# Kernel optimization log

Measured on AMD Instinct MI355X. Metric: run time of the kernel, lower is better.

## Reference

```python
import jax, jax.numpy as jnp
import numpy as np

B, S, D, H = 2, 2048, 1024, 16
DH = D // H


def setup_inputs() -> dict:
    key = jax.random.key(0)
    ks = jax.random.split(key, 13)
    def lin(kw, kb):
        w = jax.random.normal(kw, (D, D), dtype=jnp.float32) * (1.0 / np.sqrt(D))
        b = jax.random.normal(kb, (D,), dtype=jnp.float32) * 0.01
        return w, b
    wq_w, wq_b = lin(ks[0], ks[1])
    wk_w, wk_b = lin(ks[2], ks[3])
    wv_w, wv_b = lin(ks[4], ks[5])
    dense_w, dense_b = lin(ks[6], ks[7])
    q = jax.random.normal(ks[8], (B, S, D), dtype=jnp.float32)
    k = jax.random.normal(ks[9], (B, S, D), dtype=jnp.float32)
    v = jax.random.normal(ks[10], (B, S, D), dtype=jnp.float32)
    mask = jax.random.randint(ks[11], (B, 1, S, S), 0, 2, dtype=jnp.int32)
    return {"q": q, "k": k, "v": v, "mask": mask,
            "wq_w": wq_w, "wq_b": wq_b, "wk_w": wk_w, "wk_b": wk_b,
            "wv_w": wv_w, "wv_b": wv_b, "dense_w": dense_w, "dense_b": dense_b}


def _split_heads(x):
    # [B,S,D] -> [B,H,S,DH]
    b, s, _ = x.shape
    return x.reshape(b, s, H, DH).transpose(0, 2, 1, 3)


def reference(q, k, v, mask, wq_w, wq_b, wk_w, wk_b, wv_w, wv_b, dense_w, dense_b):
    qs = _split_heads(q @ wq_w.T + wq_b)
    ks = _split_heads(k @ wk_w.T + wk_b)
    vs = _split_heads(v @ wv_w.T + wv_b)
    scale = 1.0 / np.sqrt(float(DH))
    scores = jnp.einsum('bhqd,bhkd->bhqk', qs, ks) * scale  # [B,H,S,S]
    scores = jnp.where(mask == 0, -jnp.inf, scores)
    weights = jax.nn.softmax(scores, axis=-1)
    out = jnp.einsum('bhqk,bhkd->bhqd', weights, vs)
    out = out.transpose(0, 2, 1, 3).reshape(q.shape[0], -1, D)  # merge heads
    out = out @ dense_w.T + dense_b
    return (out, weights)
```

## Files before the change

kernel.cpp:

```cpp
#include <hip/hip_runtime.h>
#include <math.h>

#define Bb 2
#define Ss 2048
#define Dd 1024
#define Hh 16
#define DHh 64

typedef unsigned short u16;
typedef unsigned int u32;
typedef __attribute__((ext_vector_type(8))) short short8;
typedef __attribute__((ext_vector_type(4))) float f32x4;

#define LOG2E 1.44269504088896340736f

__device__ __forceinline__ u16 fb(float f){
    u32 x = __float_as_uint(f);
    return (u16)((x + 0x7fffu + ((x>>16)&1u)) >> 16);
}
__device__ __forceinline__ float bf2f(u16 h){
    return __uint_as_float((u32)h << 16);
}

__global__ __launch_bounds__(256) void split_hilo(
    const float* __restrict__ x, u16* __restrict__ hi, u16* __restrict__ lo,
    int n8)
{
    const int i = blockIdx.x*256 + threadIdx.x;
    if (i >= n8) return;
    float4 a = ((const float4*)x)[i*2];
    float4 b = ((const float4*)x)[i*2+1];
    float f[8] = {a.x,a.y,a.z,a.w,b.x,b.y,b.z,b.w};
    u16 h8[8], l8[8];
    #pragma unroll
    for (int j=0;j<8;j++){
        u16 h = fb(f[j]);
        h8[j] = h;
        l8[j] = fb(f[j] - bf2f(h));
    }
    *(uint4*)(hi + (size_t)i*8) = *(const uint4*)h8;
    *(uint4*)(lo + (size_t)i*8) = *(const uint4*)l8;
}

template<int MODE, int NTERM>
__global__ __launch_bounds__(256) void gemm_fused(
    const u16* __restrict__ A0, const u16* __restrict__ A1,
    const u16* __restrict__ W0, const u16* __restrict__ W1,
    const float* __restrict__ bias, void* __restrict__ outv,
    int M, int N, int K)
{
    const int t = threadIdx.x, lane = t & 63, wave = t >> 6;
    const int lr = lane & 15, lg = lane >> 4;
    const int bm = blockIdx.x, bn = blockIdx.y;
    const int wr = wave >> 1, wc = wave & 1;
    const int am0 = bm*128 + wr*64;
    const int wn0 = bn*128 + wc*64;

    const u16* P0 = (MODE==2) ? W0 : A0;
    const u16* P1 = (MODE==2) ? W1 : A1;
    const u16* Q0 = (MODE==2) ? A0 : W0;
    const u16* Q1 = (MODE==2) ? A1 : W1;
    const int pr0 = (MODE==2) ? wn0 : am0;
    const int qr0_ = (MODE==2) ? am0 : wn0;
    const u16* Pb0 = P0 + (size_t)(pr0 + lr)*K + lg*8;
    const u16* Pb1 = P1 + (size_t)(pr0 + lr)*K + lg*8;
    const u16* Qb0 = Q0 + (size_t)(qr0_ + lr)*K + lg*8;
    const u16* Qb1 = Q1 + (size_t)(qr0_ + lr)*K + lg*8;

    f32x4 acc[4][4];
    #pragma unroll
    for (int i=0;i<4;i++)
        #pragma unroll
        for (int j=0;j<4;j++){ f32x4 z={0.f,0.f,0.f,0.f}; acc[i][j]=z; }

    for (int kt=0; kt<K; kt+=32){
        short8 pf0[4], pf1[4], qf0[4], qf1[4];
        #pragma unroll
        for (int i=0;i<4;i++){
            pf0[i] = *(const short8*)(Pb0 + (size_t)(i*16)*K + kt);
            qf0[i] = *(const short8*)(Qb0 + (size_t)(i*16)*K + kt);
            qf1[i] = *(const short8*)(Qb1 + (size_t)(i*16)*K + kt);
            if (NTERM==3)
                pf1[i] = *(const short8*)(Pb1 + (size_t)(i*16)*K + kt);
        }
        #pragma unroll
        for (int i=0;i<4;i++)
            #pragma unroll
            for (int j=0;j<4;j++){
                acc[i][j] = __builtin_amdgcn_mfma_f32_16x16x32_bf16(
                    pf0[i], qf0[j], acc[i][j], 0,0,0);
                acc[i][j] = __builtin_amdgcn_mfma_f32_16x16x32_bf16(
                    pf0[i], qf1[j], acc[i][j], 0,0,0);
                if (NTERM==3)
                    acc[i][j] = __builtin_amdgcn_mfma_f32_16x16x32_bf16(
                        pf1[i], qf0[j], acc[i][j], 0,0,0);
            }
    }

    if (MODE==0){
        float* op = (float*)outv;
        float bq[4];
        #pragma unroll
        for (int j=0;j<4;j++) bq[j] = bias[wn0 + j*16 + lr];
        #pragma unroll
        for (int i=0;i<4;i++)
            #pragma unroll
            for (int r=0;r<4;r++){
                const int m = am0 + i*16 + lg*4 + r;
                #pragma unroll
                for (int j=0;j<4;j++)
                    op[(size_t)m*N + wn0 + j*16 + lr] = acc[i][j][r] + bq[j];
            }
    } else if (MODE==1){
        u16* op = (u16*)outv;
        float bq[4];
        #pragma unroll
        for (int j=0;j<4;j++) bq[j] = bias[wn0 + j*16 + lr];
        #pragma unroll
        for (int i=0;i<4;i++)
            #pragma unroll
            for (int r=0;r<4;r++){
                const int m = am0 + i*16 + lg*4 + r;
                const int b = m >> 11, s = m & (Ss-1);
                #pragma unroll
                for (int j=0;j<4;j++){
                    const int n = wn0 + j*16 + lr;
                    const int h = n >> 6, d = n & (DHh-1);
                    op[((size_t)((b*Hh + h)*Ss + s))*DHh + d] =
                        fb(acc[i][j][r] + bq[j]);
                }
            }
    } else {
        u16* op = (u16*)outv;
        float bp[4][4];
        #pragma unroll
        for (int i=0;i<4;i++){
            float4 bv = *(const float4*)(bias + wn0 + i*16 + lg*4);
            bp[i][0]=bv.x; bp[i][1]=bv.y; bp[i][2]=bv.z; bp[i][3]=bv.w;
        }
        #pragma unroll
        for (int i=0;i<4;i++)
            #pragma unroll
            for (int r=0;r<4;r++){
                const int n = wn0 + i*16 + lg*4 + r;
                const int h = n >> 6, d = n & (DHh-1);
                #pragma unroll
                for (int j=0;j<4;j++){
                    const int m = am0 + j*16 + lr;
                    const int b = m >> 11, s = m & (Ss-1);
                    op[((size_t)((b*Hh + h)*DHh + d))*Ss + s] =
                        fb(acc[i][j][r] + bp[i][r]);
                }
            }
    }
}

__global__ __launch_bounds__(256) void mask_pack(
    const int* __restrict__ mask, u32* __restrict__ mbits)
{
    const size_t w = (size_t)blockIdx.x*256 + threadIdx.x;
    const int* p = mask + w*32;
    u32 bits = 0;
    #pragma unroll
    for (int i=0;i<32;i+=4){
        int4 v = *(const int4*)(p + i);
        bits |= (u32)(v.x!=0) << i;
        bits |= (u32)(v.y!=0) << (i+1);
        bits |= (u32)(v.z!=0) << (i+2);
        bits |= (u32)(v.w!=0) << (i+3);
    }
    mbits[w] = bits;
}

__global__ __launch_bounds__(256) void attn_stats_mfma(
    const u16* __restrict__ Q, const u16* __restrict__ K,
    const u32* __restrict__ mbits,
    float* __restrict__ mstat, float* __restrict__ lstat)
{
    const int t = threadIdx.x;
    const int lane = t & 63, wave = t >> 6;
    const int qt = blockIdx.x, bh = blockIdx.y;
    const int b = bh >> 4;
    const int qr0 = qt*128 + wave*32;
    const u16* qb = Q + ((size_t)bh*Ss + qr0)*DHh;
    const u16* kb = K + (size_t)bh*Ss*DHh;
    const u32* mb = mbits + (size_t)b*Ss*(Ss/32);

    const int lr = lane & 15;
    const int lg = lane >> 4;

    short8 aq[2][2];
    #pragma unroll
    for (int s2=0;s2<2;s2++)
        #pragma unroll
        for (int dh=0; dh<2; dh++)
            aq[s2][dh] = *(const short8*)(qb + (size_t)(s2*16 + lr)*DHh + dh*32 + lg*8);

    int qv[8];
    #pragma unroll
    for (int idx=0; idx<8; idx++)
        qv[idx] = qr0 + (idx>>2)*16 + lg*4 + (idx&3);

    float m[8], l[8];
    #pragma unroll
    for (int i=0;i<8;i++){ m[i]=-1e30f; l[i]=0.f; }

    const float SC = 0.125f * LOG2E;

    for (int k0=0; k0<Ss; k0+=32){
        u32 mw[8];
        #pragma unroll
        for (int idx=0; idx<8; idx++)
            mw[idx] = mb[(size_t)qv[idx]*(Ss/32) + (k0>>5)];
        #pragma unroll
        for (int h2=0; h2<2; h2++){
            const u16* kr = kb + (size_t)(k0 + h2*16 + lr)*DHh + lg*8;
            short8 b0 = *(const short8*)kr;
            short8 b1 = *(const short8*)(kr + 32);
            f32x4 z = {0.f,0.f,0.f,0.f};
            f32x4 s0 = __builtin_amdgcn_mfma_f32_16x16x32_bf16(aq[0][0], b0, z, 0,0,0);
            s0 = __builtin_amdgcn_mfma_f32_16x16x32_bf16(aq[0][1], b1, s0, 0,0,0);
            f32x4 s1 = __builtin_amdgcn_mfma_f32_16x16x32_bf16(aq[1][0], b0, z, 0,0,0);
            s1 = __builtin_amdgcn_mfma_f32_16x16x32_bf16(aq[1][1], b1, s1, 0,0,0);
            #pragma unroll
            for (int idx=0; idx<8; idx++){
                const int s2 = idx>>2, r = idx&3;
                float sc = (s2 ? s1[r] : s0[r]) * SC;
                float x  = ((mw[idx] >> (h2*16 + lr)) & 1) ? sc : -INFINITY;
                float mo = m[idx];
                float mn = fmaxf(mo, x);
                float e  = exp2f(fminf(mo, x) - mn);
                bool gt  = x > mo;
                l[idx] = fmaf(l[idx], gt ? e : 1.f, gt ? 1.f : e);
                m[idx] = mn;
            }
        }
    }

    #pragma unroll
    for (int idx=0; idx<8; idx++){
        float mm = m[idx], ll = l[idx];
        #pragma unroll
        for (int off=1; off<16; off<<=1){
            float mo = __shfl_xor(mm, off, 64);
            float lo = __shfl_xor(ll, off, 64);
            float mn = fmaxf(mm, mo);
            ll = ll*exp2f(mm-mn) + lo*exp2f(mo-mn);
            mm = mn;
        }
        if (lr == 0){
            mstat[(size_t)bh*Ss + qv[idx]] = mm;
            lstat[(size_t)bh*Ss + qv[idx]] = ll;
        }
    }
}

__global__ __launch_bounds__(256) void attn_wpv(
    const u16* __restrict__ Q, const u16* __restrict__ K,
    const u16* __restrict__ Vt, const u32* __restrict__ mbits,
    const float* __restrict__ mstat, const float* __restrict__ lstat,
    float* __restrict__ wout, u16* __restrict__ attn)
{
    __shared__ __align__(16) u16 plds[4][32][40];
    const int t = threadIdx.x;
    const int lane = t & 63, wave = t >> 6;
    const int qt = blockIdx.x, bh = blockIdx.y;
    const int b = bh >> 4, h = bh & 15;
    const int qr0 = qt*128 + wave*32;
    const u16* qb  = Q  + ((size_t)bh*Ss + qr0)*DHh;
    const u16* kb  = K  + (size_t)bh*Ss*DHh;
    const u16* vtb = Vt + (size_t)bh*DHh*Ss;
    const u32* mb  = mbits + (size_t)b*Ss*(Ss/32);
    float* wop = wout + (size_t)bh*Ss*Ss;

    const int lr = lane & 15;
    const int lg = lane >> 4;

    short8 aq[2][2];
    #pragma unroll
    for (int s2=0;s2<2;s2++)
        #pragma unroll
        for (int dh=0; dh<2; dh++)
            aq[s2][dh] = *(const short8*)(qb + (size_t)(s2*16 + lr)*DHh + dh*32 + lg*8);

    int qv[8];
    float mrow[8], li[8];
    #pragma unroll
    for (int idx=0; idx<8; idx++){
        qv[idx] = qr0 + (idx>>2)*16 + lg*4 + (idx&3);
        mrow[idx] = mstat[(size_t)bh*Ss + qv[idx]];
        float lv  = lstat[(size_t)bh*Ss + qv[idx]];
        li[idx] = lv > 0.f ? 1.f/lv : 0.f;
    }

    f32x4 acc_o[2][4];
    #pragma unroll
    for (int s2=0;s2<2;s2++)
        #pragma unroll
        for (int dt=0;dt<4;dt++){
            f32x4 z = {0.f,0.f,0.f,0.f};
            acc_o[s2][dt] = z;
        }

    const float SC = 0.125f * LOG2E;

    for (int k0=0; k0<Ss; k0+=32){
        u32 mw[8];
        #pragma unroll
        for (int idx=0; idx<8; idx++)
            mw[idx] = mb[(size_t)qv[idx]*(Ss/32) + (k0>>5)];
        #pragma unroll
        for (int h2=0; h2<2; h2++){
            const int kk = k0 + h2*16;
            const u16* kr = kb + (size_t)(kk + lr)*DHh + lg*8;
            short8 b0 = *(const short8*)kr;
            short8 b1 = *(const short8*)(kr + 32);
            f32x4 z = {0.f,0.f,0.f,0.f};
            f32x4 s0 = __builtin_amdgcn_mfma_f32_16x16x32_bf16(aq[0][0], b0, z, 0,0,0);
            s0 = __builtin_amdgcn_mfma_f32_16x16x32_bf16(aq[0][1], b1, s0, 0,0,0);
            f32x4 s1 = __builtin_amdgcn_mfma_f32_16x16x32_bf16(aq[1][0], b0, z, 0,0,0);
            s1 = __builtin_amdgcn_mfma_f32_16x16x32_bf16(aq[1][1], b1, s1, 0,0,0);
            #pragma unroll
            for (int idx=0; idx<8; idx++){
                const int s2 = idx>>2, r = idx&3;
                float sc  = (s2 ? s1[r] : s0[r]) * SC;
                float wgt = ((mw[idx] >> (h2*16 + lr)) & 1)
                          ? exp2f(sc - mrow[idx]) * li[idx] : 0.f;
                __builtin_nontemporal_store(wgt, wop + (size_t)qv[idx]*Ss + kk + lr);
                plds[wave][s2*16 + lg*4 + r][h2*16 + lr] = fb(wgt);
            }
        }
        short8 pa0 = *(const short8*)&plds[wave][lr][lg*8];
        short8 pa1 = *(const short8*)&plds[wave][16 + lr][lg*8];
        #pragma unroll
        for (int dt=0; dt<4; dt++){
            short8 vb = *(const short8*)(vtb + (size_t)(dt*16 + lr)*Ss + k0 + lg*8);
            acc_o[0][dt] = __builtin_amdgcn_mfma_f32_16x16x32_bf16(pa0, vb, acc_o[0][dt], 0,0,0);
            acc_o[1][dt] = __builtin_amdgcn_mfma_f32_16x16x32_bf16(pa1, vb, acc_o[1][dt], 0,0,0);
        }
    }

    u16* ab = attn + (size_t)b*Ss*Dd + (size_t)h*DHh;
    #pragma unroll
    for (int s2=0;s2<2;s2++)
        #pragma unroll
        for (int dt=0;dt<4;dt++)
            #pragma unroll
            for (int r=0;r<4;r++){
                const int q = qr0 + s2*16 + lg*4 + r;
                ab[(size_t)q*Dd + dt*16 + lr] = fb(acc_o[s2][dt][r]);
            }
}

extern "C" void kernel_launch(void* const* d_in, const int* in_sizes, int n_in,
                              void* d_out, int out_size, void* d_ws, size_t ws_size,
                              hipStream_t stream) {
    const float* q      = (const float*)d_in[0];
    const float* k      = (const float*)d_in[1];
    const float* v      = (const float*)d_in[2];
    const int*   mask   = (const int*)d_in[3];
    const float* wq_w   = (const float*)d_in[4];
    const float* wq_b   = (const float*)d_in[5];
    const float* wk_w   = (const float*)d_in[6];
    const float* wk_b   = (const float*)d_in[7];
    const float* wv_w   = (const float*)d_in[8];
    const float* wv_b   = (const float*)d_in[9];
    const float* dense_w= (const float*)d_in[10];
    const float* dense_b= (const float*)d_in[11];

    float* out  = (float*)d_out;
    float* wout = out + (size_t)Bb*Ss*Dd;

    u16* qs   = (u16*)d_ws;
    u16* ksb  = qs  + (size_t)Bb*Hh*Ss*DHh;
    u16* vt   = ksb + (size_t)Bb*Hh*Ss*DHh;
    u16* attn = vt  + (size_t)Bb*Hh*Ss*DHh;
    float* mstat = (float*)(attn + (size_t)Bb*Ss*Dd);
    float* lstat = mstat + (size_t)Bb*Hh*Ss;
    u32* mbits = (u32*)(lstat + (size_t)Bb*Hh*Ss);

    u16* Ahi = (u16*)wout;
    u16* Alo = Ahi + (size_t)Bb*Ss*Dd;
    u16* Whi = Alo + (size_t)Bb*Ss*Dd;
    u16* Wlo = Whi + (size_t)Dd*Dd;
    u16* Whi2 = qs;
    u16* Wlo2 = qs + (size_t)Dd*Dd;

    const int M = Bb*Ss, N = Dd, K = Dd;
    const int n8_in = M*K/8, n8_w = N*K/8;
    dim3 gg(M/128, N/128), bb(256);

    mask_pack<<<dim3((Bb*Ss*Ss/32)/256), bb, 0, stream>>>(mask, mbits);

    split_hilo<<<dim3((n8_in+255)/256), bb, 0, stream>>>(q, Ahi, Alo, n8_in);
    split_hilo<<<dim3((n8_w+255)/256),  bb, 0, stream>>>(wq_w, Whi, Wlo, n8_w);
    gemm_fused<1,3><<<gg, bb, 0, stream>>>(Ahi, Alo, Whi, Wlo, wq_b, qs, M, N, K);
    split_hilo<<<dim3((n8_in+255)/256), bb, 0, stream>>>(k, Ahi, Alo, n8_in);
    split_hilo<<<dim3((n8_w+255)/256),  bb, 0, stream>>>(wk_w, Whi, Wlo, n8_w);
    gemm_fused<1,3><<<gg, bb, 0, stream>>>(Ahi, Alo, Whi, Wlo, wk_b, ksb, M, N, K);
    split_hilo<<<dim3((n8_in+255)/256), bb, 0, stream>>>(v, Ahi, Alo, n8_in);
    split_hilo<<<dim3((n8_w+255)/256),  bb, 0, stream>>>(wv_w, Whi, Wlo, n8_w);
    gemm_fused<2,3><<<gg, bb, 0, stream>>>(Ahi, Alo, Whi, Wlo, wv_b, vt, M, N, K);

    dim3 ga(Ss/128, Bb*Hh);
    attn_stats_mfma<<<ga, bb, 0, stream>>>(qs, ksb, mbits, mstat, lstat);
    attn_wpv      <<<ga, bb, 0, stream>>>(qs, ksb, vt, mbits, mstat, lstat, wout, attn);

    split_hilo<<<dim3((n8_w+255)/256), bb, 0, stream>>>(dense_w, Whi2, Wlo2, n8_w);
    gemm_fused<0,2><<<gg, bb, 0, stream>>>(attn, attn, Whi2, Wlo2, dense_b, out, M, N, K);
}
```

Baseline: 1.114 ms.

## Batch QKV splits and projections into single launches, retile dense GEMM

Six hi/lo split kernels become one batched launch. The three QKV projection GEMMs become one grid of 3×8 column blocks per row tile, which triples the blocks in flight and cuts launch gaps. The dense projection moves to its own kernel with 128×64 tiles, doubling its block count for better CU occupancy. Staging buffers now hold all three split inputs at once inside the weights output region, which raises scratch footprint.

```diff
diff --git a/kernel.cpp b/kernel.cpp
--- a/kernel.cpp
+++ b/kernel.cpp
@@ -20,6 +20,28 @@
 }
 __device__ __forceinline__ float bf2f(u16 h){
     return __uint_as_float((u32)h << 16);
+}
+
+struct SplitJob { const float* src; u16* hi; u16* lo; int n8; };
+struct SplitJobs { SplitJob j[6]; };
+
+__global__ __launch_bounds__(256) void split_batch(SplitJobs jobs)
+{
+    const SplitJob J = jobs.j[blockIdx.y];
+    const int i = blockIdx.x*256 + threadIdx.x;
+    if (i >= J.n8) return;
+    float4 a = ((const float4*)J.src)[i*2];
+    float4 b = ((const float4*)J.src)[i*2+1];
+    float f[8] = {a.x,a.y,a.z,a.w,b.x,b.y,b.z,b.w};
+    u16 h8[8], l8[8];
+    #pragma unroll
+    for (int j=0;j<8;j++){
+        u16 h = fb(f[j]);
+        h8[j] = h;
+        l8[j] = fb(f[j] - bf2f(h));
+    }
+    *(uint4*)(J.hi + (size_t)i*8) = *(const uint4*)h8;
+    *(uint4*)(J.lo + (size_t)i*8) = *(const uint4*)l8;
 }
 
 __global__ __launch_bounds__(256) void split_hilo(
@@ -42,30 +64,43 @@
     *(uint4*)(lo + (size_t)i*8) = *(const uint4*)l8;
 }
 
-template<int MODE, int NTERM>
-__global__ __launch_bounds__(256) void gemm_fused(
-    const u16* __restrict__ A0, const u16* __restrict__ A1,
-    const u16* __restrict__ W0, const u16* __restrict__ W1,
-    const float* __restrict__ bias, void* __restrict__ outv,
-    int M, int N, int K)
-{
+__global__ __launch_bounds__(256, 3) void gemm_qkv(
+    const u16* __restrict__ qh, const u16* __restrict__ ql,
+    const u16* __restrict__ kh, const u16* __restrict__ kl,
+    const u16* __restrict__ vh, const u16* __restrict__ vl,
+    const u16* __restrict__ wqh, const u16* __restrict__ wql,
+    const u16* __restrict__ wkh, const u16* __restrict__ wkl,
+    const u16* __restrict__ wvh, const u16* __restrict__ wvl,
+    const float* __restrict__ bq, const float* __restrict__ bk,
+    const float* __restrict__ bv,
+    u16* __restrict__ qs, u16* __restrict__ ksb, u16* __restrict__ vt)
+{
+    const int K = Dd;
     const int t = threadIdx.x, lane = t & 63, wave = t >> 6;
     const int lr = lane & 15, lg = lane >> 4;
-    const int bm = blockIdx.x, bn = blockIdx.y;
+    const int bm = blockIdx.x;
+    const int proj = blockIdx.y >> 3, bnn = blockIdx.y & 7;
     const int wr = wave >> 1, wc = wave & 1;
     const int am0 = bm*128 + wr*64;
-    const int wn0 = bn*128 + wc*64;
-
-    const u16* P0 = (MODE==2) ? W0 : A0;
-    const u16* P1 = (MODE==2) ? W1 : A1;
-    const u16* Q0 = (MODE==2) ? A0 : W0;
-    const u16* Q1 = (MODE==2) ? A1 : W1;
-    const int pr0 = (MODE==2) ? wn0 : am0;
-    const int qr0_ = (MODE==2) ? am0 : wn0;
-    const u16* Pb0 = P0 + (size_t)(pr0 + lr)*K + lg*8;
-    const u16* Pb1 = P1 + (size_t)(pr0 + lr)*K + lg*8;
-    const u16* Qb0 = Q0 + (size_t)(qr0_ + lr)*K + lg*8;
-    const u16* Qb1 = Q1 + (size_t)(qr0_ + lr)*K + lg*8;
+    const int wn0 = bnn*128 + wc*64;
+
+    const u16* Ah = proj==0 ? qh : proj==1 ? kh : vh;
+    const u16* Al = proj==0 ? ql : proj==1 ? kl : vl;
+    const u16* Wh = proj==0 ? wqh : proj==1 ? wkh : wvh;
+    const u16* Wl = proj==0 ? wql : proj==1 ? wkl : wvl;
+    const float* bias = proj==0 ? bq : proj==1 ? bk : bv;
+
+    const bool swap = (proj==2);
+    const u16* P0 = swap ? Wh : Ah;
+    const u16* P1 = swap ? Wl : Al;
+    const u16* Q0 = swap ? Ah : Wh;
+    const u16* Q1 = swap ? Al : Wl;
+    const int prow = swap ? wn0 : am0;
+    const int qrow = swap ? am0 : wn0;
+    const u16* Pb0 = P0 + (size_t)(prow + lr)*K + lg*8;
+    const u16* Pb1 = P1 + (size_t)(prow + lr)*K + lg*8;
+    const u16* Qb0 = Q0 + (size_t)(qrow + lr)*K + lg*8;
+    const u16* Qb1 = Q1 + (size_t)(qrow + lr)*K + lg*8;
 
     f32x4 acc[4][4];
     #pragma unroll
@@ -80,8 +115,7 @@
             pf0[i] = *(const short8*)(Pb0 + (size_t)(i*16)*K + kt);
             qf0[i] = *(const short8*)(Qb0 + (size_t)(i*16)*K + kt);
             qf1[i] = *(const short8*)(Qb1 + (size_t)(i*16)*K + kt);
-            if (NTERM==3)
-                pf1[i] = *(const short8*)(Pb1 + (size_t)(i*16)*K + kt);
+            pf1[i] = *(const short8*)(Pb1 + (size_t)(i*16)*K + kt);
         }
         #pragma unroll
         for (int i=0;i<4;i++)
@@ -91,31 +125,16 @@
                     pf0[i], qf0[j], acc[i][j], 0,0,0);
                 acc[i][j] = __builtin_amdgcn_mfma_f32_16x16x32_bf16(
                     pf0[i], qf1[j], acc[i][j], 0,0,0);
-                if (NTERM==3)
-                    acc[i][j] = __builtin_amdgcn_mfma_f32_16x16x32_bf16(
-                        pf1[i], qf0[j], acc[i][j], 0,0,0);
-            }
-    }
-
-    if (MODE==0){
-        float* op = (float*)outv;
-        float bq[4];
-        #pragma unroll
-        for (int j=0;j<4;j++) bq[j] = bias[wn0 + j*16 + lr];
-        #pragma unroll
-        for (int i=0;i<4;i++)
-            #pragma unroll
-            for (int r=0;r<4;r++){
-                const int m = am0 + i*16 + lg*4 + r;
-                #pragma unroll
-                for (int j=0;j<4;j++)
-                    op[(size_t)m*N + wn0 + j*16 + lr] = acc[i][j][r] + bq[j];
-            }
-    } else if (MODE==1){
-        u16* op = (u16*)outv;
-        float bq[4];
-        #pragma unroll
-        for (int j=0;j<4;j++) bq[j] = bias[wn0 + j*16 + lr];
+                acc[i][j] = __builtin_amdgcn_mfma_f32_16x16x32_bf16(
+                    pf1[i], qf0[j], acc[i][j], 0,0,0);
+            }
+    }
+
+    if (!swap){
+        u16* op = proj==0 ? qs : ksb;
+        float bq4[4];
+        #pragma unroll
+        for (int j=0;j<4;j++) bq4[j] = bias[wn0 + j*16 + lr];
         #pragma unroll
         for (int i=0;i<4;i++)
             #pragma unroll
@@ -127,16 +146,15 @@
                     const int n = wn0 + j*16 + lr;
                     const int h = n >> 6, d = n & (DHh-1);
                     op[((size_t)((b*Hh + h)*Ss + s))*DHh + d] =
-                        fb(acc[i][j][r] + bq[j]);
+                        fb(acc[i][j][r] + bq4[j]);
                 }
             }
     } else {
-        u16* op = (u16*)outv;
         float bp[4][4];
         #pragma unroll
         for (int i=0;i<4;i++){
-            float4 bv = *(const float4*)(bias + wn0 + i*16 + lg*4);
-            bp[i][0]=bv.x; bp[i][1]=bv.y; bp[i][2]=bv.z; bp[i][3]=bv.w;
+            float4 bvv = *(const float4*)(bias + wn0 + i*16 + lg*4);
+            bp[i][0]=bvv.x; bp[i][1]=bvv.y; bp[i][2]=bvv.z; bp[i][3]=bvv.w;
         }
         #pragma unroll
         for (int i=0;i<4;i++)
@@ -148,11 +166,69 @@
                 for (int j=0;j<4;j++){
                     const int m = am0 + j*16 + lr;
                     const int b = m >> 11, s = m & (Ss-1);
-                    op[((size_t)((b*Hh + h)*DHh + d))*Ss + s] =
+                    vt[((size_t)((b*Hh + h)*DHh + d))*Ss + s] =
                         fb(acc[i][j][r] + bp[i][r]);
                 }
             }
     }
+}
+
+__global__ __launch_bounds__(256) void gemm_dense(
+    const u16* __restrict__ A, const u16* __restrict__ W0,
+    const u16* __restrict__ W1, const float* __restrict__ bias,
+    float* __restrict__ out)
+{
+    const int K = Dd, N = Dd;
+    const int t = threadIdx.x, lane = t & 63, wave = t >> 6;
+    const int lr = lane & 15, lg = lane >> 4;
+    const int bm = blockIdx.x, bn = blockIdx.y;
+    const int wr = wave >> 1, wc = wave & 1;
+    const int am0 = bm*128 + wr*64;
+    const int wn0 = bn*64 + wc*32;
+
+    const u16* Pb0 = A  + (size_t)(am0 + lr)*K + lg*8;
+    const u16* Qb0 = W0 + (size_t)(wn0 + lr)*K + lg*8;
+    const u16* Qb1 = W1 + (size_t)(wn0 + lr)*K + lg*8;
+
+    f32x4 acc[4][2];
+    #pragma unroll
+    for (int i=0;i<4;i++)
+        #pragma unroll
+        for (int j=0;j<2;j++){ f32x4 z={0.f,0.f,0.f,0.f}; acc[i][j]=z; }
+
+    for (int kt=0; kt<K; kt+=32){
+        short8 pf0[4], qf0[2], qf1[2];
+        #pragma unroll
+        for (int i=0;i<4;i++)
+            pf0[i] = *(const short8*)(Pb0 + (size_t)(i*16)*K + kt);
+        #pragma unroll
+        for (int j=0;j<2;j++){
+            qf0[j] = *(const short8*)(Qb0 + (size_t)(j*16)*K + kt);
+            qf1[j] = *(const short8*)(Qb1 + (size_t)(j*16)*K + kt);
+        }
+        #pragma unroll
+        for (int i=0;i<4;i++)
+            #pragma unroll
+            for (int j=0;j<2;j++){
+                acc[i][j] = __builtin_amdgcn_mfma_f32_16x16x32_bf16(
+                    pf0[i], qf0[j], acc[i][j], 0,0,0);
+                acc[i][j] = __builtin_amdgcn_mfma_f32_16x16x32_bf16(
+                    pf0[i], qf1[j], acc[i][j], 0,0,0);
+            }
+    }
+
+    float bq[2];
+    #pragma unroll
+    for (int j=0;j<2;j++) bq[j] = bias[wn0 + j*16 + lr];
+    #pragma unroll
+    for (int i=0;i<4;i++)
+        #pragma unroll
+        for (int r=0;r<4;r++){
+            const int m = am0 + i*16 + lg*4 + r;
+            #pragma unroll
+            for (int j=0;j<2;j++)
+                out[(size_t)m*N + wn0 + j*16 + lr] = acc[i][j][r] + bq[j];
+        }
 }
 
 __global__ __launch_bounds__(256) void mask_pack(
@@ -379,33 +455,41 @@
     float* lstat = mstat + (size_t)Bb*Hh*Ss;
     u32* mbits = (u32*)(lstat + (size_t)Bb*Hh*Ss);
 
-    u16* Ahi = (u16*)wout;
-    u16* Alo = Ahi + (size_t)Bb*Ss*Dd;
-    u16* Whi = Alo + (size_t)Bb*Ss*Dd;
-    u16* Wlo = Whi + (size_t)Dd*Dd;
+    const size_t NA = (size_t)Bb*Ss*Dd;
+    const size_t NW = (size_t)Dd*Dd;
+    u16* SB  = (u16*)wout;
+    u16* qhi = SB;            u16* qlo = qhi + NA;
+    u16* khi = qlo + NA;      u16* klo = khi + NA;
+    u16* vhi = klo + NA;      u16* vlo = vhi + NA;
+    u16* wqh = vlo + NA;      u16* wql = wqh + NW;
+    u16* wkh = wql + NW;      u16* wkl = wkh + NW;
+    u16* wvh = wkl + NW;      u16* wvl = wvh + NW;
     u16* Whi2 = qs;
-    u16* Wlo2 = qs + (size_t)Dd*Dd;
-
-    const int M = Bb*Ss, N = Dd, K = Dd;
-    const int n8_in = M*K/8, n8_w = N*K/8;
-    dim3 gg(M/128, N/128), bb(256);
+    u16* Wlo2 = qs + NW;
+
+    const int M = Bb*Ss;
+    const int n8A = (int)(NA/8), n8W = (int)(NW/8);
+    dim3 bb(256);
 
     mask_pack<<<dim3((Bb*Ss*Ss/32)/256), bb, 0, stream>>>(mask, mbits);
 
-    split_hilo<<<dim3((n8_in+255)/256), bb, 0, stream>>>(q, Ahi, Alo, n8_in);
-    split_hilo<<<dim3((n8_w+255)/256),  bb, 0, stream>>>(wq_w, Whi, Wlo, n8_w);
-    gemm_fused<1,3><<<gg, bb, 0, stream>>>(Ahi, Alo, Whi, Wlo, wq_b, qs, M, N, K);
-    split_hilo<<<dim3((n8_in+255)/256), bb, 0, stream>>>(k, Ahi, Alo, n8_in);
-    split_hilo<<<dim3((n8_w+255)/256),  bb, 0, stream>>>(wk_w, Whi, Wlo, n8_w);
-    gemm_fused<1,3><<<gg, bb, 0, stream>>>(Ahi, Alo, Whi, Wlo, wk_b, ksb, M, N, K);
-    split_hilo<<<dim3((n8_in+255)/256), bb, 0, stream>>>(v, Ahi, Alo, n8_in);
-    split_hilo<<<dim3((n8_w+255)/256),  bb, 0, stream>>>(wv_w, Whi, Wlo, n8_w);
-    gemm_fused<2,3><<<gg, bb, 0, stream>>>(Ahi, Alo, Whi, Wlo, wv_b, vt, M, N, K);
+    SplitJobs jobs;
+    jobs.j[0] = { q,    qhi, qlo, n8A };
+    jobs.j[1] = { k,    khi, klo, n8A };
+    jobs.j[2] = { v,    vhi, vlo, n8A };
+    jobs.j[3] = { wq_w, wqh, wql, n8W };
+    jobs.j[4] = { wk_w, wkh, wkl, n8W };
+    jobs.j[5] = { wv_w, wvh, wvl, n8W };
+    split_batch<<<dim3(n8A/256, 6), bb, 0, stream>>>(jobs);
+
+    gemm_qkv<<<dim3(M/128, 24), bb, 0, stream>>>(
+        qhi,qlo, khi,klo, vhi,vlo, wqh,wql, wkh,wkl, wvh,wvl,
+        wq_b, wk_b, wv_b, qs, ksb, vt);
 
     dim3 ga(Ss/128, Bb*Hh);
     attn_stats_mfma<<<ga, bb, 0, stream>>>(qs, ksb, mbits, mstat, lstat);
     attn_wpv      <<<ga, bb, 0, stream>>>(qs, ksb, vt, mbits, mstat, lstat, wout, attn);
 
-    split_hilo<<<dim3((n8_w+255)/256), bb, 0, stream>>>(dense_w, Whi2, Wlo2, n8_w);
-    gemm_fused<0,2><<<gg, bb, 0, stream>>>(attn, attn, Whi2, Wlo2, dense_b, out, M, N, K);
-}
+    split_hilo<<<dim3((n8W+255)/256), bb, 0, stream>>>(dense_w, Whi2, Wlo2, n8W);
+    gemm_dense<<<dim3(M/128, Dd/64), bb, 0, stream>>>(attn, Whi2, Wlo2, dense_b, out);
+}
```

Result: faster. 1.081 ms (-3.0%).
